# Kernel optimization log

Hardware: AMD Instinct MI355X
Metric: run time of the kernel (lower is better)

The kernel has to match this reference:

```python
import jax, jax.numpy as jnp
import numpy as np

# dims
B, T, H = 4, 2048, 768
HEADS, D = 4, 768          # GATConv(out_channels=768, heads=4, concat=False)
L = 3                      # num_layers
WIN = 2
K = 2 * WIN + 1
EPS = 1e-5
NEG_SLOPE = 0.2            # PyG GATConv leaky_relu slope


def setup_inputs() -> dict:
    key = jax.random.key(0)
    ks = jax.random.split(key, 4)
    s = 1.0 / np.sqrt(H)
    x = jax.random.normal(ks[0], (B, T, H), jnp.float32)
    W = jax.random.normal(ks[1], (L, H, HEADS, D), jnp.float32) * s   # lin weights per layer
    a_src = jax.random.normal(ks[2], (L, HEADS, D), jnp.float32) * s  # att_src
    a_dst = jax.random.normal(ks[3], (L, HEADS, D), jnp.float32) * s  # att_dst
    bias = jnp.zeros((L, D), jnp.float32)                             # GATConv bias (concat=False -> [D])
    gamma = jnp.ones((L, H), jnp.float32)                             # LayerNorm weight
    beta = jnp.zeros((L, H), jnp.float32)                             # LayerNorm bias
    return {"x": x, "W": W, "a_src": a_src, "a_dst": a_dst,
            "bias": bias, "gamma": gamma, "beta": beta}


def _layernorm(z, g, b):
    m = jnp.mean(z, axis=-1, keepdims=True)
    v = jnp.mean((z - m) ** 2, axis=-1, keepdims=True)
    return (z - m) * jax.lax.rsqrt(v + EPS) * g + b


def _gat_layer(x, Wl, asrc_w, adst_w, bias_l, idx, mask):
    # x: [B,T,H]; banded GAT with neighborhoods idx: [T,K] (clipped), mask: [T,K]
    h = jnp.einsum('bti,ihd->bthd', x, Wl)                 # [B,T,heads,D]
    asrc = jnp.einsum('bthd,hd->bth', h, asrc_w)           # per-source-node score term
    adst = jnp.einsum('bthd,hd->bth', h, adst_w)           # per-target-node score term
    h_nb = h[:, idx]                                       # [B,T,K,heads,D] gathered neighbors j
    score = jax.nn.leaky_relu(asrc[:, idx] + adst[:, :, None, :], NEG_SLOPE)  # [B,T,K,heads]
    score = jnp.where(mask[None, :, :, None], score, -jnp.inf)
    attn = jax.nn.softmax(score, axis=2)                   # softmax over incoming edges per target
    out = jnp.einsum('btkh,btkhd->bthd', attn, h_nb)       # weighted aggregation
    return out.mean(axis=2) + bias_l                       # concat=False -> mean over heads


def reference(x, W, a_src, a_dst, bias, gamma, beta):
    # banded neighborhood indices (window edges both directions + self-loop from PyG default)
    offs = jnp.arange(-WIN, WIN + 1)
    idx = jnp.arange(T)[:, None] + offs[None, :]           # [T,K]
    mask = (idx >= 0) & (idx < T)
    idx = jnp.clip(idx, 0, T - 1)
    for l in range(L):
        res = x
        y = _gat_layer(x, W[l], a_src[l], a_dst[l], bias[l], idx, mask)
        x = _layernorm(y + res, gamma[l], beta[l])         # dropout = identity in eval
    return x
```

## Files before the change

kernel.cpp:

```cpp
#include <hip/hip_runtime.h>
#include <stdint.h>

#define TT 2048
#define BB 4
#define HH 768
#define NHEADS 4
#define DD 768
#define NN 3072
#define LL 3
#define BT 8192
#define KNB 5
#define NBLK 12
#define ATPB 4
#define NROWS 8

typedef __bf16 bf16x8 __attribute__((ext_vector_type(8)));
typedef float f32x4 __attribute__((ext_vector_type(4)));

__device__ __forceinline__ unsigned short f2bf(float f){
  union { float f; unsigned u; } v; v.f = f;
  unsigned u = v.u;
  return (unsigned short)((u + 0x7FFFu + ((u >> 16) & 1u)) >> 16);
}
__device__ __forceinline__ float bf2f(unsigned short h){
  union { unsigned u; float f; } v; v.u = ((unsigned)h) << 16;
  return v.f;
}
__device__ __forceinline__ void gload16(const unsigned short* g, unsigned short* l){
  __builtin_amdgcn_global_load_lds((const __attribute__((address_space(1))) void*)g,
                                   (__attribute__((address_space(3))) void*)l, 16, 0, 0);
}

__global__ void wt_kernel(const float* __restrict__ W, unsigned short* __restrict__ Wt){
  __shared__ float tile[32][33];
  int l = blockIdx.z;
  int n0 = blockIdx.x * 32, k0 = blockIdx.y * 32;
  int tx = threadIdx.x, ty = threadIdx.y;
  const float* Wl = W + (size_t)l * HH * NN;
  for (int r = 0; r < 4; r++)
    tile[ty + r*8][tx] = Wl[(size_t)(k0 + ty + r*8) * NN + n0 + tx];
  __syncthreads();
  unsigned short* Wtl = Wt + (size_t)l * NN * HH;
  for (int r = 0; r < 4; r++){
    int n = n0 + ty + r*8;
    Wtl[(size_t)n * HH + k0 + tx] = f2bf(tile[tx][ty + r*8]);
  }
}

__global__ void xconv_kernel(const float* __restrict__ x, unsigned short* __restrict__ xb){
  int i = blockIdx.x * blockDim.x + threadIdx.x;
  float4 v = ((const float4*)x)[i];
  ushort4 o;
  o.x = f2bf(v.x); o.y = f2bf(v.y); o.z = f2bf(v.z); o.w = f2bf(v.w);
  *(ushort4*)(xb + (size_t)i * 4) = o;
}

#define BM 128
#define BN 128
#define BK 64

__global__ __launch_bounds__(256, 3) void gemm_kernel(
    const unsigned short* __restrict__ xb,
    const unsigned short* __restrict__ wt,
    unsigned short* __restrict__ hout,
    const float* __restrict__ a_srcl,
    const float* __restrict__ a_dstl,
    float* __restrict__ psrc,
    float* __restrict__ pdst){
  __shared__ __align__(16) unsigned short xs[BM][BK];
  __shared__ __align__(16) unsigned short wsd[BN][BK];
  int id = blockIdx.x;
  int xcd = id & 7;
  int s = id >> 3;
  int bn_i = s / 8;
  int bm_i = (s & 7) + xcd * 8;
  int bm = bm_i * BM;
  int bn = bn_i * BN;
  int tid = threadIdx.x;
  int wave = tid >> 6, lane = tid & 63;
  int m16 = lane & 15, q = lane >> 4;
  int wm = (wave >> 1) * 64, wn = (wave & 1) * 64;
  int r8 = lane >> 3, c8 = lane & 7;
  int cg = (c8 ^ r8) * 8;
  const unsigned short* ga[4]; const unsigned short* gb[4];
  unsigned short* la[4]; unsigned short* lb[4];
  #pragma unroll
  for (int ss = 0; ss < 4; ss++){
    int row = wave * 32 + ss * 8;
    ga[ss] = xb + (size_t)(bm + row + r8) * HH + cg;
    gb[ss] = wt + (size_t)(bn + row + r8) * HH + cg;
    la[ss] = &xs[row][0];
    lb[ss] = &wsd[row][0];
  }
  int rd0 = ((0 + q) ^ (m16 & 7)) * 8;
  int rd1 = ((4 + q) ^ (m16 & 7)) * 8;
  f32x4 acc[4][4] = {};
  for (int k0 = 0; k0 < HH; k0 += BK){
    #pragma unroll
    for (int ss = 0; ss < 4; ss++){
      gload16(ga[ss] + k0, la[ss]);
      gload16(gb[ss] + k0, lb[ss]);
    }
    __syncthreads();
    bf16x8 af[4], bfr[4];
    for (int i = 0; i < 4; i++)
      af[i] = __builtin_bit_cast(bf16x8, *(const uint4*)(&xs[wm + i*16 + m16][rd0]));
    for (int j = 0; j < 4; j++)
      bfr[j] = __builtin_bit_cast(bf16x8, *(const uint4*)(&wsd[wn + j*16 + m16][rd0]));
    for (int i = 0; i < 4; i++)
      for (int j = 0; j < 4; j++)
        acc[i][j] = __builtin_amdgcn_mfma_f32_16x16x32_bf16(af[i], bfr[j], acc[i][j], 0, 0, 0);
    for (int i = 0; i < 4; i++)
      af[i] = __builtin_bit_cast(bf16x8, *(const uint4*)(&xs[wm + i*16 + m16][rd1]));
    for (int j = 0; j < 4; j++)
      bfr[j] = __builtin_bit_cast(bf16x8, *(const uint4*)(&wsd[wn + j*16 + m16][rd1]));
    for (int i = 0; i < 4; i++)
      for (int j = 0; j < 4; j++)
        acc[i][j] = __builtin_amdgcn_mfma_f32_16x16x32_bf16(af[i], bfr[j], acc[i][j], 0, 0, 0);
    __syncthreads();
  }
  for (int i = 0; i < 4; i++){
    int row0 = bm + wm + i*16 + q*4;
    for (int j = 0; j < 4; j++){
      int col = bn + wn + j*16 + m16;
      unsigned short* hp = hout + (size_t)row0 * NN + col;
      hp[0]            = f2bf(acc[i][j][0]);
      hp[NN]           = f2bf(acc[i][j][1]);
      hp[2*(size_t)NN] = f2bf(acc[i][j][2]);
      hp[3*(size_t)NN] = f2bf(acc[i][j][3]);
    }
  }
  int col0 = bn + wn;
  int head = col0 / DD;
  int blk  = (col0 % DD) >> 6;
  float wsrc[4], wdstw[4];
  for (int j = 0; j < 4; j++){
    int n = col0 + j*16 + m16;
    wsrc[j]  = a_srcl[n];
    wdstw[j] = a_dstl[n];
  }
  for (int i = 0; i < 4; i++){
    for (int reg = 0; reg < 4; reg++){
      float ss = 0.f, dd = 0.f;
      for (int j = 0; j < 4; j++){
        float v = acc[i][j][reg];
        ss += v * wsrc[j];
        dd += v * wdstw[j];
      }
      ss += __shfl_xor(ss, 1, 64); dd += __shfl_xor(dd, 1, 64);
      ss += __shfl_xor(ss, 2, 64); dd += __shfl_xor(dd, 2, 64);
      ss += __shfl_xor(ss, 4, 64); dd += __shfl_xor(dd, 4, 64);
      ss += __shfl_xor(ss, 8, 64); dd += __shfl_xor(dd, 8, 64);
      if (m16 == 0){
        int row = bm + wm + i*16 + q*4 + reg;
        size_t slot = (size_t)row * (NHEADS * NBLK) + head * NBLK + blk;
        psrc[slot] = ss;
        pdst[slot] = dd;
      }
    }
  }
}

__global__ __launch_bounds__(384) void attn_ln_kernel(const unsigned short* __restrict__ h,
    const float* __restrict__ psrc, const float* __restrict__ pdst,
    const float* __restrict__ xin_f32,
    const unsigned short* __restrict__ xin_bf,
    const float* __restrict__ bias_l,
    const float* __restrict__ gamma_l, const float* __restrict__ beta_l,
    float* __restrict__ x_out, unsigned short* __restrict__ xb_next,
    int write_f32){
  int bid = blockIdx.x;
  int grp = ((bid & 7) << 8) | (bid >> 3);
  int token0 = grp * ATPB;
  int t0 = token0 & (TT - 1);
  int bseq = token0 >> 11;
  int tid = threadIdx.x;
  int wave = tid >> 6, lane = tid & 63;
  int ti = tid / 96, c = tid % 96;
  int token = token0 + ti;
  __shared__ __align__(16) unsigned short hs[NROWS][NN];
  __shared__ float attn_s[ATPB][NHEADS][KNB];
  __shared__ float as_sh[NROWS * NHEADS], ad_sh[NROWS * NHEADS];
  __shared__ float part_s[ATPB * 96], part_q[ATPB * 96];
  __shared__ float mv_mean[ATPB], mv_rstd[ATPB];
  #pragma unroll
  for (int j = 0; j < NROWS; j++){
    int g = t0 - 2 + j;
    g = min(max(g, 0), TT - 1);
    const unsigned short* src = h + ((size_t)(bseq * TT + g)) * NN + tid * 8;
    gload16(src, &hs[j][wave * 512]);
  }
  float xr[8], bb[8], gr[8], br[8];
  if (xin_f32){
    const float4* p = (const float4*)&xin_f32[(size_t)token * HH + c * 8];
    *(float4*)&xr[0] = p[0]; *(float4*)&xr[4] = p[1];
  } else {
    uint4 u = *(const uint4*)&xin_bf[(size_t)token * HH + c * 8];
    const unsigned short* us = (const unsigned short*)&u;
    #pragma unroll
    for (int e = 0; e < 8; e++) xr[e] = bf2f(us[e]);
  }
  { const float4* p = (const float4*)&bias_l[c * 8];
    *(float4*)&bb[0] = p[0]; *(float4*)&bb[4] = p[1]; }
  { const float4* p = (const float4*)&gamma_l[c * 8];
    *(float4*)&gr[0] = p[0]; *(float4*)&gr[4] = p[1]; }
  { const float4* p = (const float4*)&beta_l[c * 8];
    *(float4*)&br[0] = p[0]; *(float4*)&br[4] = p[1]; }
  if (tid < 2 * NROWS * NHEADS){
    int which = tid >= NROWS * NHEADS;
    int i = tid & (NROWS * NHEADS - 1);
    int lt = i >> 2, head = i & 3;
    int tcl = min(max(t0 - 2 + lt, 0), TT - 1);
    const float* p = (which ? pdst : psrc) +
        ((size_t)(bseq * TT + tcl) * NHEADS + head) * NBLK;
    float4 a = *(const float4*)(p);
    float4 b = *(const float4*)(p + 4);
    float4 d = *(const float4*)(p + 8);
    float s = a.x+a.y+a.z+a.w + b.x+b.y+b.z+b.w + d.x+d.y+d.z+d.w;
    (which ? ad_sh : as_sh)[i] = s;
  }
  __syncthreads();
  if (tid < ATPB * NHEADS){
    int tii = tid >> 2, head = tid & 3;
    int t = t0 + tii;
    float sc[KNB];
    float mx = -3.0e38f;
    float ad = ad_sh[(tii + 2) * NHEADS + head];
    for (int k = 0; k < KNB; k++){
      int tn = t + k - 2;
      if (tn >= 0 && tn < TT){
        float s = as_sh[(tii + k) * NHEADS + head] + ad;
        s = s > 0.f ? s : 0.2f * s;
        sc[k] = s; mx = fmaxf(mx, s);
      } else sc[k] = -3.0e38f;
    }
    float den = 0.f;
    for (int k = 0; k < KNB; k++){
      float e = (sc[k] > -1.0e38f) ? __expf(sc[k] - mx) : 0.f;
      sc[k] = e; den += e;
    }
    float inv = 0.25f / den;
    for (int k = 0; k < KNB; k++) attn_s[tii][head][k] = sc[k] * inv;
  }
  __syncthreads();
  float ac[NHEADS][KNB];
  for (int hd = 0; hd < NHEADS; hd++)
    for (int k = 0; k < KNB; k++) ac[hd][k] = attn_s[ti][hd][k];
  float y8[8] = {};
  for (int hd = 0; hd < NHEADS; hd++){
    #pragma unroll
    for (int k = 0; k < KNB; k++){
      bf16x8 v = __builtin_bit_cast(bf16x8, *(const uint4*)(&hs[ti + k][hd * DD + c * 8]));
      float a = ac[hd][k];
      #pragma unroll
      for (int e = 0; e < 8; e++) y8[e] += a * (float)v[e];
    }
  }
  float s = 0.f, sq = 0.f;
  #pragma unroll
  for (int e = 0; e < 8; e++){
    float zz = y8[e] + bb[e] + xr[e];
    y8[e] = zz; s += zz; sq += zz * zz;
  }
  part_s[tid] = s; part_q[tid] = sq;
  __syncthreads();
  if (wave < ATPB){
    float vs = part_s[wave * 96 + lane];
    float vq = part_q[wave * 96 + lane];
    if (lane < 32){
      vs += part_s[wave * 96 + 64 + lane];
      vq += part_q[wave * 96 + 64 + lane];
    }
    for (int off = 32; off > 0; off >>= 1){
      vs += __shfl_xor(vs, off, 64);
      vq += __shfl_xor(vq, off, 64);
    }
    if (lane == 0){
      float mean = vs * (1.f / HH);
      float var = vq * (1.f / HH) - mean * mean;
      mv_mean[wave] = mean;
      mv_rstd[wave] = rsqrtf(var + 1e-5f);
    }
  }
  __syncthreads();
  float mean = mv_mean[ti], rstd = mv_rstd[ti];
  float o[8];
  #pragma unroll
  for (int e = 0; e < 8; e++)
    o[e] = (y8[e] - mean) * rstd * gr[e] + br[e];
  if (write_f32){
    float* xo = &x_out[(size_t)token * HH + c * 8];
    *(float4*)&xo[0] = *(float4*)&o[0];
    *(float4*)&xo[4] = *(float4*)&o[4];
  } else {
    unsigned short o16[8];
    #pragma unroll
    for (int e = 0; e < 8; e++) o16[e] = f2bf(o[e]);
    *(uint4*)(&xb_next[(size_t)token * HH + c * 8]) = *(uint4*)&o16[0];
  }
}

extern "C" void kernel_launch(void* const* d_in, const int* in_sizes, int n_in,
                              void* d_out, int out_size, void* d_ws, size_t ws_size,
                              hipStream_t stream) {
  const float* x     = (const float*)d_in[0];
  const float* W     = (const float*)d_in[1];
  const float* a_src = (const float*)d_in[2];
  const float* a_dst = (const float*)d_in[3];
  const float* bias  = (const float*)d_in[4];
  const float* gamma = (const float*)d_in[5];
  const float* beta  = (const float*)d_in[6];
  float* out = (float*)d_out;

  char* ws = (char*)d_ws;
  size_t off = 0;
  auto alloc = [&](size_t bytes)->char*{
    char* p = ws + off;
    off = (off + bytes + 255) & ~(size_t)255;
    return p;
  };
  unsigned short* wt   = (unsigned short*)alloc((size_t)LL * NN * HH * 2);
  unsigned short* xb   = (unsigned short*)alloc((size_t)BT * HH * 2);
  unsigned short* hbuf = (unsigned short*)alloc((size_t)BT * NN * 2);
  float* psrc  = (float*)alloc((size_t)BT * NHEADS * NBLK * 4);
  float* pdst  = (float*)alloc((size_t)BT * NHEADS * NBLK * 4);

  wt_kernel<<<dim3(NN/32, HH/32, LL), dim3(32, 8), 0, stream>>>(W, wt);
  xconv_kernel<<<(BT * HH / 4) / 256, 256, 0, stream>>>(x, xb);

  for (int l = 0; l < LL; l++){
    gemm_kernel<<<(NN / BN) * (BT / BM), 256, 0, stream>>>(
        xb, wt + (size_t)l * NN * HH, hbuf,
        a_src + (size_t)l * NHEADS * DD, a_dst + (size_t)l * NHEADS * DD,
        psrc, pdst);
    attn_ln_kernel<<<BT / ATPB, 384, 0, stream>>>(hbuf, psrc, pdst,
        (l == 0) ? x : nullptr, xb,
        bias + (size_t)l * DD, gamma + (size_t)l * HH, beta + (size_t)l * HH,
        out, xb, (l == LL - 1) ? 1 : 0);
  }
}
```

Before: 329.7 us.

## Rewrite projection GEMM as 256x256 double-buffered tile with interleaved prefetch

The projection GEMM moves from 128x128 tiles with 4 waves to 256x256 tiles with 8 waves and a double-buffered LDS. Next-tile global-to-LDS loads are split into quarters and interleaved with the MFMA phases, using explicit waitcnt, barriers and setprio. The aim is to hide global load latency behind compute and raise data reuse per block. In exchange it uses more LDS and registers (two blocks per CU) and launches fewer blocks (384 vs 1536), which could cost occupancy or expose tail effects.

```diff
diff --git a/kernel.cpp b/kernel.cpp
--- a/kernel.cpp
+++ b/kernel.cpp
@@ -29,6 +29,14 @@
 __device__ __forceinline__ void gload16(const unsigned short* g, unsigned short* l){
   __builtin_amdgcn_global_load_lds((const __attribute__((address_space(1))) void*)g,
                                    (__attribute__((address_space(3))) void*)l, 16, 0, 0);
+}
+__device__ __forceinline__ bf16x8 ld16(const unsigned short* p){
+  return __builtin_bit_cast(bf16x8, *(const uint4*)p);
+}
+__device__ __forceinline__ void fencebar(){
+  asm volatile("" ::: "memory");
+  __builtin_amdgcn_s_barrier();
+  asm volatile("" ::: "memory");
 }
 
 __global__ void wt_kernel(const float* __restrict__ W, unsigned short* __restrict__ Wt){
@@ -55,11 +63,12 @@
   *(ushort4*)(xb + (size_t)i * 4) = o;
 }
 
-#define BM 128
-#define BN 128
+#define BM 256
+#define BN 256
 #define BK 64
-
-__global__ __launch_bounds__(256, 3) void gemm_kernel(
+#define NKT (HH / BK)
+
+__global__ __launch_bounds__(512, 2) void gemm_kernel(
     const unsigned short* __restrict__ xb,
     const unsigned short* __restrict__ wt,
     unsigned short* __restrict__ hout,
@@ -67,62 +76,137 @@
     const float* __restrict__ a_dstl,
     float* __restrict__ psrc,
     float* __restrict__ pdst){
-  __shared__ __align__(16) unsigned short xs[BM][BK];
-  __shared__ __align__(16) unsigned short wsd[BN][BK];
+  __shared__ __align__(16) unsigned short As[2][BM][BK];
+  __shared__ __align__(16) unsigned short Bs[2][BN][BK];
   int id = blockIdx.x;
   int xcd = id & 7;
   int s = id >> 3;
-  int bn_i = s / 8;
-  int bm_i = (s & 7) + xcd * 8;
+  int bn_i = s >> 2;
+  int bm_i = xcd * 4 + (s & 3);
   int bm = bm_i * BM;
   int bn = bn_i * BN;
   int tid = threadIdx.x;
   int wave = tid >> 6, lane = tid & 63;
   int m16 = lane & 15, q = lane >> 4;
-  int wm = (wave >> 1) * 64, wn = (wave & 1) * 64;
+  int wm = wave >> 2, wn = wave & 3;
   int r8 = lane >> 3, c8 = lane & 7;
   int cg = (c8 ^ r8) * 8;
-  const unsigned short* ga[4]; const unsigned short* gb[4];
-  unsigned short* la[4]; unsigned short* lb[4];
+
+  const unsigned short* gA[4]; const unsigned short* gB[4];
+  int arow[4], brow[4];
   #pragma unroll
   for (int ss = 0; ss < 4; ss++){
-    int row = wave * 32 + ss * 8;
-    ga[ss] = xb + (size_t)(bm + row + r8) * HH + cg;
-    gb[ss] = wt + (size_t)(bn + row + r8) * HH + cg;
-    la[ss] = &xs[row][0];
-    lb[ss] = &wsd[row][0];
+    int o = wave * 2 + (ss & 1);
+    arow[ss] = (ss >> 1) * 64 + o * 8 + ((o >= 8) ? 64 : 0);
+    brow[ss] = wave * 32 + ss * 8;
+    gA[ss] = xb + (size_t)(bm + arow[ss] + r8) * HH + cg;
+    gB[ss] = wt + (size_t)(bn + brow[ss] + r8) * HH + cg;
   }
   int rd0 = ((0 + q) ^ (m16 & 7)) * 8;
   int rd1 = ((4 + q) ^ (m16 & 7)) * 8;
-  f32x4 acc[4][4] = {};
-  for (int k0 = 0; k0 < HH; k0 += BK){
-    #pragma unroll
-    for (int ss = 0; ss < 4; ss++){
-      gload16(ga[ss] + k0, la[ss]);
-      gload16(gb[ss] + k0, lb[ss]);
-    }
-    __syncthreads();
-    bf16x8 af[4], bfr[4];
+  f32x4 acc[8][4] = {};
+
+  #pragma unroll
+  for (int ss = 0; ss < 4; ss++) gload16(gB[ss], &Bs[0][brow[ss]][0]);
+  #pragma unroll
+  for (int ss = 0; ss < 4; ss++) gload16(gA[ss], &As[0][arow[ss]][0]);
+  asm volatile("s_waitcnt vmcnt(2)" ::: "memory");
+  fencebar();
+
+  #pragma unroll 2
+  for (int kt = 0; kt < NKT; kt++){
+    int cur = kt & 1, nxt = cur ^ 1;
+    int koff = (kt + 1) * BK;
+    bf16x8 af[4], bfv[4];
+    #pragma unroll
     for (int i = 0; i < 4; i++)
-      af[i] = __builtin_bit_cast(bf16x8, *(const uint4*)(&xs[wm + i*16 + m16][rd0]));
+      af[i] = ld16(&As[cur][wm*128 + i*16 + m16][rd0]);
+    #pragma unroll
     for (int j = 0; j < 4; j++)
-      bfr[j] = __builtin_bit_cast(bf16x8, *(const uint4*)(&wsd[wn + j*16 + m16][rd0]));
+      bfv[j] = ld16(&Bs[cur][wn*64 + j*16 + m16][rd0]);
+    if (kt < NKT-1){
+      gload16(gB[0] + koff, &Bs[nxt][brow[0]][0]);
+      gload16(gB[1] + koff, &Bs[nxt][brow[1]][0]);
+    }
+    fencebar();
+    asm volatile("s_waitcnt lgkmcnt(0)" ::: "memory");
+    __builtin_amdgcn_s_setprio(1);
+    #pragma unroll
+    for (int i = 0; i < 4; i++){
+      #pragma unroll
+      for (int j = 0; j < 4; j++)
+        acc[i][j] = __builtin_amdgcn_mfma_f32_16x16x32_bf16(af[i], bfv[j], acc[i][j], 0, 0, 0);
+    }
+    __builtin_amdgcn_s_setprio(0);
+    if (kt < NKT-1) { asm volatile("s_waitcnt vmcnt(2)" ::: "memory"); }
+    else            { asm volatile("s_waitcnt vmcnt(0)" ::: "memory"); }
+    fencebar();
+    #pragma unroll
     for (int i = 0; i < 4; i++)
+      af[i] = ld16(&As[cur][wm*128 + 64 + i*16 + m16][rd0]);
+    if (kt < NKT-1){
+      gload16(gB[2] + koff, &Bs[nxt][brow[2]][0]);
+      gload16(gB[3] + koff, &Bs[nxt][brow[3]][0]);
+    }
+    fencebar();
+    asm volatile("s_waitcnt lgkmcnt(0)" ::: "memory");
+    __builtin_amdgcn_s_setprio(1);
+    #pragma unroll
+    for (int i = 0; i < 4; i++){
+      #pragma unroll
       for (int j = 0; j < 4; j++)
-        acc[i][j] = __builtin_amdgcn_mfma_f32_16x16x32_bf16(af[i], bfr[j], acc[i][j], 0, 0, 0);
+        acc[4+i][j] = __builtin_amdgcn_mfma_f32_16x16x32_bf16(af[i], bfv[j], acc[4+i][j], 0, 0, 0);
+    }
+    __builtin_amdgcn_s_setprio(0);
+    fencebar();
+    #pragma unroll
     for (int i = 0; i < 4; i++)
-      af[i] = __builtin_bit_cast(bf16x8, *(const uint4*)(&xs[wm + i*16 + m16][rd1]));
+      af[i] = ld16(&As[cur][wm*128 + i*16 + m16][rd1]);
+    #pragma unroll
     for (int j = 0; j < 4; j++)
-      bfr[j] = __builtin_bit_cast(bf16x8, *(const uint4*)(&wsd[wn + j*16 + m16][rd1]));
+      bfv[j] = ld16(&Bs[cur][wn*64 + j*16 + m16][rd1]);
+    if (kt < NKT-1){
+      gload16(gA[0] + koff, &As[nxt][arow[0]][0]);
+      gload16(gA[1] + koff, &As[nxt][arow[1]][0]);
+    }
+    fencebar();
+    asm volatile("s_waitcnt lgkmcnt(0)" ::: "memory");
+    __builtin_amdgcn_s_setprio(1);
+    #pragma unroll
+    for (int i = 0; i < 4; i++){
+      #pragma unroll
+      for (int j = 0; j < 4; j++)
+        acc[i][j] = __builtin_amdgcn_mfma_f32_16x16x32_bf16(af[i], bfv[j], acc[i][j], 0, 0, 0);
+    }
+    __builtin_amdgcn_s_setprio(0);
+    fencebar();
+    #pragma unroll
     for (int i = 0; i < 4; i++)
+      af[i] = ld16(&As[cur][wm*128 + 64 + i*16 + m16][rd1]);
+    if (kt < NKT-1){
+      gload16(gA[2] + koff, &As[nxt][arow[2]][0]);
+      gload16(gA[3] + koff, &As[nxt][arow[3]][0]);
+    }
+    fencebar();
+    asm volatile("s_waitcnt lgkmcnt(0)" ::: "memory");
+    __builtin_amdgcn_s_setprio(1);
+    #pragma unroll
+    for (int i = 0; i < 4; i++){
+      #pragma unroll
       for (int j = 0; j < 4; j++)
-        acc[i][j] = __builtin_amdgcn_mfma_f32_16x16x32_bf16(af[i], bfr[j], acc[i][j], 0, 0, 0);
-    __syncthreads();
-  }
-  for (int i = 0; i < 4; i++){
-    int row0 = bm + wm + i*16 + q*4;
+        acc[4+i][j] = __builtin_amdgcn_mfma_f32_16x16x32_bf16(af[i], bfv[j], acc[4+i][j], 0, 0, 0);
+    }
+    __builtin_amdgcn_s_setprio(0);
+    if (kt < NKT-1) { asm volatile("s_waitcnt vmcnt(2)" ::: "memory"); }
+    fencebar();
+  }
+
+  #pragma unroll
+  for (int i = 0; i < 8; i++){
+    int row0 = bm + wm*128 + i*16 + q*4;
+    #pragma unroll
     for (int j = 0; j < 4; j++){
-      int col = bn + wn + j*16 + m16;
+      int col = bn + wn*64 + j*16 + m16;
       unsigned short* hp = hout + (size_t)row0 * NN + col;
       hp[0]            = f2bf(acc[i][j][0]);
       hp[NN]           = f2bf(acc[i][j][1]);
@@ -130,18 +214,22 @@
       hp[3*(size_t)NN] = f2bf(acc[i][j][3]);
     }
   }
-  int col0 = bn + wn;
+  int col0 = bn + wn*64;
   int head = col0 / DD;
   int blk  = (col0 % DD) >> 6;
   float wsrc[4], wdstw[4];
+  #pragma unroll
   for (int j = 0; j < 4; j++){
     int n = col0 + j*16 + m16;
     wsrc[j]  = a_srcl[n];
     wdstw[j] = a_dstl[n];
   }
-  for (int i = 0; i < 4; i++){
+  #pragma unroll
+  for (int i = 0; i < 8; i++){
+    #pragma unroll
     for (int reg = 0; reg < 4; reg++){
       float ss = 0.f, dd = 0.f;
+      #pragma unroll
       for (int j = 0; j < 4; j++){
         float v = acc[i][j][reg];
         ss += v * wsrc[j];
@@ -152,7 +240,7 @@
       ss += __shfl_xor(ss, 4, 64); dd += __shfl_xor(dd, 4, 64);
       ss += __shfl_xor(ss, 8, 64); dd += __shfl_xor(dd, 8, 64);
       if (m16 == 0){
-        int row = bm + wm + i*16 + q*4 + reg;
+        int row = bm + wm*128 + i*16 + q*4 + reg;
         size_t slot = (size_t)row * (NHEADS * NBLK) + head * NBLK + blk;
         psrc[slot] = ss;
         pdst[slot] = dd;
@@ -329,7 +417,7 @@
   xconv_kernel<<<(BT * HH / 4) / 256, 256, 0, stream>>>(x, xb);
 
   for (int l = 0; l < LL; l++){
-    gemm_kernel<<<(NN / BN) * (BT / BM), 256, 0, stream>>>(
+    gemm_kernel<<<(BT / BM) * (NN / BN), 512, 0, stream>>>(
         xb, wt + (size_t)l * NN * HH, hbuf,
         a_src + (size_t)l * NHEADS * DD, a_dst + (size_t)l * NHEADS * DD,
         psrc, pdst);
```

Result: slower. 438.4 us (+33.0%).

## Drop LDS staging of h rows; read neighbors directly from global

Applied to the files above, without the earlier changes.

The attention/LayerNorm kernel no longer stages eight neighbor rows of h into a 48KB shared buffer. Each thread now reads its five neighbor rows straight from global memory and relies on cache for reuse across tokens. The softmax weights are also computed redundantly in every thread, which removes one barrier and the attn_s shared array. This lowers LDS use, which should allow more blocks per CU. The cost is more global and L2 traffic, since overlapping rows are fetched repeatedly by different tokens.

```diff
diff --git a/kernel.cpp b/kernel.cpp
--- a/kernel.cpp
+++ b/kernel.cpp
@@ -178,34 +178,10 @@
   int wave = tid >> 6, lane = tid & 63;
   int ti = tid / 96, c = tid % 96;
   int token = token0 + ti;
-  __shared__ __align__(16) unsigned short hs[NROWS][NN];
-  __shared__ float attn_s[ATPB][NHEADS][KNB];
   __shared__ float as_sh[NROWS * NHEADS], ad_sh[NROWS * NHEADS];
   __shared__ float part_s[ATPB * 96], part_q[ATPB * 96];
   __shared__ float mv_mean[ATPB], mv_rstd[ATPB];
-  #pragma unroll
-  for (int j = 0; j < NROWS; j++){
-    int g = t0 - 2 + j;
-    g = min(max(g, 0), TT - 1);
-    const unsigned short* src = h + ((size_t)(bseq * TT + g)) * NN + tid * 8;
-    gload16(src, &hs[j][wave * 512]);
-  }
-  float xr[8], bb[8], gr[8], br[8];
-  if (xin_f32){
-    const float4* p = (const float4*)&xin_f32[(size_t)token * HH + c * 8];
-    *(float4*)&xr[0] = p[0]; *(float4*)&xr[4] = p[1];
-  } else {
-    uint4 u = *(const uint4*)&xin_bf[(size_t)token * HH + c * 8];
-    const unsigned short* us = (const unsigned short*)&u;
-    #pragma unroll
-    for (int e = 0; e < 8; e++) xr[e] = bf2f(us[e]);
-  }
-  { const float4* p = (const float4*)&bias_l[c * 8];
-    *(float4*)&bb[0] = p[0]; *(float4*)&bb[4] = p[1]; }
-  { const float4* p = (const float4*)&gamma_l[c * 8];
-    *(float4*)&gr[0] = p[0]; *(float4*)&gr[4] = p[1]; }
-  { const float4* p = (const float4*)&beta_l[c * 8];
-    *(float4*)&br[0] = p[0]; *(float4*)&br[4] = p[1]; }
+
   if (tid < 2 * NROWS * NHEADS){
     int which = tid >= NROWS * NHEADS;
     int i = tid & (NROWS * NHEADS - 1);
@@ -219,39 +195,62 @@
     float s = a.x+a.y+a.z+a.w + b.x+b.y+b.z+b.w + d.x+d.y+d.z+d.w;
     (which ? ad_sh : as_sh)[i] = s;
   }
+
+  float xr[8], bb[8], gr[8], br[8];
+  if (xin_f32){
+    const float4* p = (const float4*)&xin_f32[(size_t)token * HH + c * 8];
+    *(float4*)&xr[0] = p[0]; *(float4*)&xr[4] = p[1];
+  } else {
+    uint4 u = *(const uint4*)&xin_bf[(size_t)token * HH + c * 8];
+    const unsigned short* us = (const unsigned short*)&u;
+    #pragma unroll
+    for (int e = 0; e < 8; e++) xr[e] = bf2f(us[e]);
+  }
+  { const float4* p = (const float4*)&bias_l[c * 8];
+    *(float4*)&bb[0] = p[0]; *(float4*)&bb[4] = p[1]; }
+  { const float4* p = (const float4*)&gamma_l[c * 8];
+    *(float4*)&gr[0] = p[0]; *(float4*)&gr[4] = p[1]; }
+  { const float4* p = (const float4*)&beta_l[c * 8];
+    *(float4*)&br[0] = p[0]; *(float4*)&br[4] = p[1]; }
   __syncthreads();
-  if (tid < ATPB * NHEADS){
-    int tii = tid >> 2, head = tid & 3;
-    int t = t0 + tii;
+
+  float aw[NHEADS][KNB];
+  #pragma unroll
+  for (int hd = 0; hd < NHEADS; hd++){
+    float ad = ad_sh[(ti + 2) * NHEADS + hd];
     float sc[KNB];
     float mx = -3.0e38f;
-    float ad = ad_sh[(tii + 2) * NHEADS + head];
+    #pragma unroll
     for (int k = 0; k < KNB; k++){
-      int tn = t + k - 2;
+      int tn = t0 + ti + k - 2;
       if (tn >= 0 && tn < TT){
-        float s = as_sh[(tii + k) * NHEADS + head] + ad;
+        float s = as_sh[(ti + k) * NHEADS + hd] + ad;
         s = s > 0.f ? s : 0.2f * s;
         sc[k] = s; mx = fmaxf(mx, s);
       } else sc[k] = -3.0e38f;
     }
     float den = 0.f;
+    #pragma unroll
     for (int k = 0; k < KNB; k++){
       float e = (sc[k] > -1.0e38f) ? __expf(sc[k] - mx) : 0.f;
       sc[k] = e; den += e;
     }
     float inv = 0.25f / den;
-    for (int k = 0; k < KNB; k++) attn_s[tii][head][k] = sc[k] * inv;
-  }
-  __syncthreads();
-  float ac[NHEADS][KNB];
-  for (int hd = 0; hd < NHEADS; hd++)
-    for (int k = 0; k < KNB; k++) ac[hd][k] = attn_s[ti][hd][k];
+    #pragma unroll
+    for (int k = 0; k < KNB; k++) aw[hd][k] = sc[k] * inv;
+  }
+
+  const unsigned short* hbase = h + (size_t)(bseq * TT) * NN + c * 8;
   float y8[8] = {};
-  for (int hd = 0; hd < NHEADS; hd++){
-    #pragma unroll
-    for (int k = 0; k < KNB; k++){
-      bf16x8 v = __builtin_bit_cast(bf16x8, *(const uint4*)(&hs[ti + k][hd * DD + c * 8]));
-      float a = ac[hd][k];
+  #pragma unroll
+  for (int k = 0; k < KNB; k++){
+    int g = t0 + ti + k - 2;
+    g = min(max(g, 0), TT - 1);
+    const unsigned short* hr = hbase + (size_t)g * NN;
+    #pragma unroll
+    for (int hd = 0; hd < NHEADS; hd++){
+      bf16x8 v = __builtin_bit_cast(bf16x8, *(const uint4*)(hr + hd * DD));
+      float a = aw[hd][k];
       #pragma unroll
       for (int e = 0; e < 8; e++) y8[e] += a * (float)v[e];
     }
```

Measured after the change: 339.5 us. +2.9%, slower.
